# Kernel tuning notes

Hardware: AMD Instinct MI355X
Metric: run time of the kernel (lower is better)

Reference implementation:

```python
import jax, jax.numpy as jnp
from jax import lax
import numpy as np

RADIUS = 2.0
K = 32          # max_neighbors
KNN = 3         # knn_num for FP interpolation
DEPTH = 3
NH = 16         # nhidden
NIN = 16
NOUT = 2
N = 16384
BOX = 32.0


def sqdist(a, b):
    # a: [M,3], b: [N,3] -> [M,N] squared distances (no [M,N,3] intermediate)
    d2 = (jnp.sum(a * a, -1)[:, None] + jnp.sum(b * b, -1)[None, :]
          - 2.0 * a @ b.T)
    return jnp.maximum(d2, 0.0)


def fps(pos, m):
    # farthest point sampling, deterministic start at index 0 (eval mode)
    n = pos.shape[0]
    def step(carry, _):
        mind, last = carry
        d = jnp.sum((pos - pos[last]) ** 2, axis=-1)
        mind = jnp.minimum(mind, d)
        nxt = jnp.argmax(mind).astype(jnp.int32)
        return (mind, nxt), nxt
    init = (jnp.full((n,), jnp.inf, dtype=pos.dtype), jnp.array(0, jnp.int32))
    _, rest = lax.scan(step, init, None, length=m - 1)
    return jnp.concatenate([jnp.zeros((1,), jnp.int32), rest])


def radius_group(pos_tgt, pos_src, r, k):
    # up-to-k neighbors of each target within radius r (nearest-first)
    d2 = sqdist(pos_tgt, pos_src)                      # [M,N]
    neg = jnp.where(d2 <= r * r, -d2, -jnp.inf)
    vals, cols = lax.top_k(neg, k)                     # [M,K]
    valid = jnp.isfinite(vals)
    return cols, valid


def knn_interpolate(x_c, pos_c, pos_f, k):
    d2 = sqdist(pos_f, pos_c)                          # [Nf, Nc]
    negv, nn = lax.top_k(-d2, k)                       # k nearest coarse pts
    w = 1.0 / jnp.maximum(-negv, 1e-16)
    w = w / jnp.sum(w, -1, keepdims=True)
    return jnp.sum(x_c[nn] * w[..., None], axis=1)     # [Nf, C]


def mlp2(h, W0, b0, W1, b1, act_last=True):
    h = jax.nn.relu(h @ W0 + b0)
    h = h @ W1 + b1
    return jax.nn.relu(h) if act_last else h


def setup_inputs() -> dict:
    key = jax.random.key(0)
    ks = jax.random.split(key, 24)
    s = 0.2
    dim_sa = NH + 3   # 19: PointConv concat(x_j, rel_pos)
    dim_fp = NH + NH  # 32: FP concat(interp, skip)
    return {
        "x": jax.random.normal(ks[0], (N, NIN), jnp.float32),
        "pos": jax.random.uniform(ks[1], (N, 3), jnp.float32) * BOX,
        "batch": jnp.zeros((N,), jnp.int32),
        "lin_in_W0": jax.random.normal(ks[2], (NIN, NH)) * s,
        "lin_in_b0": jnp.zeros((NH,), jnp.float32),
        "lin_in_W1": jax.random.normal(ks[3], (NH, NH)) * s,
        "lin_in_b1": jnp.zeros((NH,), jnp.float32),
        "sa_W0": jax.random.normal(ks[4], (DEPTH, dim_sa, dim_sa)) * s,
        "sa_b0": jnp.zeros((DEPTH, dim_sa), jnp.float32),
        "sa_W1": jax.random.normal(ks[5], (DEPTH, dim_sa, NH)) * s,
        "sa_b1": jnp.zeros((DEPTH, NH), jnp.float32),
        "fp_W0": jax.random.normal(ks[6], (DEPTH, dim_fp, dim_fp)) * s,
        "fp_b0": jnp.zeros((DEPTH, dim_fp), jnp.float32),
        "fp_W1": jax.random.normal(ks[7], (DEPTH, dim_fp, NH)) * s,
        "fp_b1": jnp.zeros((DEPTH, NH), jnp.float32),
        "lo_W0": jax.random.normal(ks[8], (NH, NH)) * s,
        "lo_b0": jnp.zeros((NH,), jnp.float32),
        "lo_W1": jax.random.normal(ks[9], (NH, NOUT)) * s,
        "lo_b1": jnp.zeros((NOUT,), jnp.float32),
    }


def reference(x, pos, batch,
              lin_in_W0, lin_in_b0, lin_in_W1, lin_in_b1,
              sa_W0, sa_b0, sa_W1, sa_b1,
              fp_W0, fp_b0, fp_W1, fp_b1,
              lo_W0, lo_b0, lo_W1, lo_b1):
    # lin_in MLP
    h = mlp2(x, lin_in_W0, lin_in_b0, lin_in_W1, lin_in_b1)
    sa = [(h, pos)]
    # SA (downsampling) path
    for i in range(DEPTH):
        xi, pi = sa[i]
        m = pi.shape[0] // 2                      # ratio = 0.5
        idx = fps(pi, m)
        pt = pi[idx]                              # sampled centers [M,3]
        cols, valid = radius_group(pt, pi, RADIUS, K)   # [M,K]
        xj = xi[cols]                             # [M,K,NH]
        rel = pi[cols] - pt[:, None, :]           # [M,K,3]
        msg = jnp.concatenate([xj, rel], -1)      # [M,K,19]
        msg = mlp2(msg, sa_W0[i], sa_b0[i], sa_W1[i], sa_b1[i])
        msg = jnp.where(valid[..., None], msg, -1e30)
        xn = jnp.max(msg, axis=1)                 # max aggregation (PointConv)
        sa.append((xn, pt))
    # FP (upsampling) path
    xf, pf = sa[DEPTH]
    for i in range(DEPTH - 1, -1, -1):
        xs, ps = sa[i]
        xi = knn_interpolate(xf, pf, ps, KNN)
        hcat = jnp.concatenate([xi, xs], -1)      # [Nf, 32]
        xf = mlp2(hcat, fp_W0[i], fp_b0[i], fp_W1[i], fp_b1[i])
        pf = ps
    # lin_out: relu then linear (act=['relu', None])
    return mlp2(xf, lo_W0, lo_b0, lo_W1, lo_b1, act_last=False)
```

## Files before the change

kernel.cpp:

```cpp
#include <hip/hip_runtime.h>
#include <stdint.h>


#define DEV static __device__ __forceinline__

DEV float fadd_(float a, float b){ return __fadd_rn(a,b); }
DEV float fsub_(float a, float b){ return __fsub_rn(a,b); }
DEV float fmul_(float a, float b){ return __fmul_rn(a,b); }
DEV float fdiv_(float a, float b){ return __fdiv_rn(a,b); }

DEV float dot3(float ax,float ay,float az,float bx,float by,float bz){
  return fmaf(az,bz, fmaf(ay,by, __fmul_rn(ax,bx)));
}
DEV float sqd(float na, float nb, float d){
  float t = __fadd_rn(na, nb);
  float u = __fmul_rn(2.0f, d);
  return fmaxf(__fsub_rn(t, u), 0.0f);
}

DEV float d2f_(float ax,float ay,float az,float bx,float by,float bz){
  float dx=fsub_(ax,bx), dy=fsub_(ay,by), dz=fsub_(az,bz);
  return fadd_(fadd_(fmul_(dx,dx),fmul_(dy,dy)),fmul_(dz,dz));
}
DEV float nrm3_(float x,float y,float z){
  return fadd_(fadd_(fmul_(x,x),fmul_(y,y)),fmul_(z,z));
}

DEV float bbd2(float sx,float sy,float sz,
               float lx,float ly,float lz,float hx,float hy,float hz){
  float dx = fmaxf(fmaxf(fsub_(lx,sx), fsub_(sx,hx)), 0.0f);
  float dy = fmaxf(fmaxf(fsub_(ly,sy), fsub_(sy,hy)), 0.0f);
  float dz = fmaxf(fmaxf(fsub_(lz,sz), fsub_(sz,hz)), 0.0f);
  return fadd_(fadd_(fmul_(dx,dx),fmul_(dy,dy)),fmul_(dz,dz));
}

DEV float rfl_f(float v){
  return __int_as_float(__builtin_amdgcn_readfirstlane(__float_as_int(v)));
}

#define DPP0(src, ctrl, rm, bc) \
  __builtin_amdgcn_update_dpp(0, (int)(src), (ctrl), (rm), 0xf, (bc))

#define DPP64(dst, src, ctrl, rm, bc) { \
  uint32_t lo_ = (uint32_t)DPP0((uint32_t)(src), ctrl, rm, bc); \
  uint32_t hi_ = (uint32_t)DPP0((uint32_t)((src)>>32), ctrl, rm, bc); \
  (dst) = (((unsigned long long)hi_)<<32) | lo_; }

#define MERGE4(A1,A2,A3,A4, ctrl, rm, bc) { \
  unsigned long long b1_,b2_,b3_,b4_, m1_,m2_,m3_,m4_, t_; \
  DPP64(b1_, A1, ctrl, rm, bc); \
  DPP64(b2_, A2, ctrl, rm, bc); \
  DPP64(b3_, A3, ctrl, rm, bc); \
  DPP64(b4_, A4, ctrl, rm, bc); \
  m1_ = (A1) > b4_ ? (A1) : b4_; \
  m2_ = (A2) > b3_ ? (A2) : b3_; \
  m3_ = (A3) > b2_ ? (A3) : b2_; \
  m4_ = (A4) > b1_ ? (A4) : b1_; \
  t_ = m1_ < m3_ ? m1_ : m3_;  m1_ = m1_ > m3_ ? m1_ : m3_;  m3_ = t_; \
  t_ = m2_ < m4_ ? m2_ : m4_;  m2_ = m2_ > m4_ ? m2_ : m4_;  m4_ = t_; \
  t_ = m1_ < m2_ ? m1_ : m2_;  m1_ = m1_ > m2_ ? m1_ : m2_;  m2_ = t_; \
  t_ = m3_ < m4_ ? m3_ : m4_;  m3_ = m3_ > m4_ ? m3_ : m4_;  m4_ = t_; \
  (A1)=m1_; (A2)=m2_; (A3)=m3_; (A4)=m4_; }

DEV unsigned long long rdlane64(unsigned long long v, int l){
  uint32_t lo=(uint32_t)__builtin_amdgcn_readlane((int)(uint32_t)v, l);
  uint32_t hi=(uint32_t)__builtin_amdgcn_readlane((int)(uint32_t)(v>>32), l);
  return (((unsigned long long)hi)<<32)|lo;
}

DEV void wtop4(unsigned long long &A1, unsigned long long &A2,
               unsigned long long &A3, unsigned long long &A4){
  MERGE4(A1,A2,A3,A4,0x111,0xf,true)
  MERGE4(A1,A2,A3,A4,0x112,0xf,true)
  MERGE4(A1,A2,A3,A4,0x114,0xf,true)
  MERGE4(A1,A2,A3,A4,0x118,0xf,true)
  MERGE4(A1,A2,A3,A4,0x142,0xa,false)
  MERGE4(A1,A2,A3,A4,0x143,0xc,false)
  A1 = rdlane64(A1,63); A2 = rdlane64(A2,63);
  A3 = rdlane64(A3,63); A4 = rdlane64(A4,63);
}

__global__ __launch_bounds__(256) void k_prep(
    const float* __restrict__ x, const float* __restrict__ pos,
    const float* __restrict__ W0, const float* __restrict__ b0,
    const float* __restrict__ W1, const float* __restrict__ b1,
    float4* __restrict__ pos4, float* __restrict__ h_out, int n)
{
  __shared__ float sW0[256], sb0[16], sW1[256], sb1[16];
  int tid = threadIdx.x;
  sW0[tid] = W0[tid];
  sW1[tid] = W1[tid];
  if (tid < 16){ sb0[tid] = b0[tid]; sb1[tid] = b1[tid]; }
  __syncthreads();
  int p = blockIdx.x*256 + tid;
  if (p >= n) return;

  float px = pos[3*p], py = pos[3*p+1], pz = pos[3*p+2];
  float nrm = fadd_(fadd_(fmul_(px,px), fmul_(py,py)), fmul_(pz,pz));
  pos4[p] = make_float4(px,py,pz,nrm);

  const float4* xr = (const float4*)(x + (size_t)p*16);
  float4 v0 = xr[0], v1 = xr[1], v2 = xr[2], v3 = xr[3];
  float xin[16] = {v0.x,v0.y,v0.z,v0.w, v1.x,v1.y,v1.z,v1.w,
                   v2.x,v2.y,v2.z,v2.w, v3.x,v3.y,v3.z,v3.w};
  float h1[16];
  #pragma unroll
  for (int o=0;o<16;o++){
    float acc = fmul_(xin[0], sW0[o]);
    #pragma unroll
    for (int k=1;k<16;k++) acc = fmaf(xin[k], sW0[k*16+o], acc);
    h1[o] = fmaxf(fadd_(acc, sb0[o]), 0.0f);
  }
  float h2[16];
  #pragma unroll
  for (int o=0;o<16;o++){
    float acc = fmul_(h1[0], sW1[o]);
    #pragma unroll
    for (int k=1;k<16;k++) acc = fmaf(h1[k], sW1[k*16+o], acc);
    h2[o] = fmaxf(fadd_(acc, sb1[o]), 0.0f);
  }
  float4* hw = (float4*)(h_out + (size_t)p*16);
  hw[0] = make_float4(h2[0], h2[1], h2[2], h2[3]);
  hw[1] = make_float4(h2[4], h2[5], h2[6], h2[7]);
  hw[2] = make_float4(h2[8], h2[9], h2[10],h2[11]);
  hw[3] = make_float4(h2[12],h2[13],h2[14],h2[15]);
}

DEV uint32_t expand4(uint32_t v){
  return (v&1u) | ((v&2u)<<2) | ((v&4u)<<4) | ((v&8u)<<6);
}
DEV int cellc(float v){
  int c = (int)(v*0.5f);
  return c < 0 ? 0 : (c > 15 ? 15 : c);
}
DEV uint32_t mkey(float4 p){
  return expand4((uint32_t)cellc(p.x))
       | (expand4((uint32_t)cellc(p.y))<<1)
       | (expand4((uint32_t)cellc(p.z))<<2);
}

__global__ __launch_bounds__(1024) void k_sort(
  const float4* __restrict__ nat, float4* __restrict__ srt,
  int* __restrict__ rank0, int n)
{
  __shared__ uint32_t hist[4096];
  __shared__ uint32_t gsum[1024];
  int tid = threadIdx.x;
  for (int i=tid;i<4096;i+=1024) hist[i]=0u;
  __syncthreads();
  for (int i=tid;i<n;i+=1024){
    float4 p = nat[i];
    atomicAdd(&hist[mkey(p)], 1u);
  }
  __syncthreads();
  uint32_t h0=hist[4*tid],h1=hist[4*tid+1],h2=hist[4*tid+2],h3=hist[4*tid+3];
  gsum[tid] = h0+h1+h2+h3;
  __syncthreads();
  for (int off=1; off<1024; off<<=1){
    uint32_t v = gsum[tid];
    uint32_t a = (tid>=off)? gsum[tid-off] : 0u;
    __syncthreads();
    gsum[tid] = v + a;
    __syncthreads();
  }
  uint32_t excl = (tid>0)? gsum[tid-1] : 0u;
  hist[4*tid]   = excl;
  hist[4*tid+1] = excl + h0;
  hist[4*tid+2] = excl + h0 + h1;
  hist[4*tid+3] = excl + h0 + h1 + h2;
  __syncthreads();
  for (int i=tid;i<n;i+=1024){
    float4 p = nat[i];
    uint32_t r = atomicAdd(&hist[mkey(p)], 1u);
    srt[r] = make_float4(p.x, p.y, p.z, __uint_as_float((uint32_t)i));
    if (i==0) *rank0 = (int)r;
  }
}

template<int P>
__global__ __attribute__((amdgpu_waves_per_eu(4,4)))
__launch_bounds__(1024) void k_fps7(
    const float4* __restrict__ sp4,
    const int* __restrict__ rank0p,
    float4* __restrict__ samp,
    int m)
{
  __shared__ float smind[P*1024];
  __shared__ unsigned long long xch[2][64];
  const int t = threadIdx.x;
  const int lane = t & 63;
  const int w = t >> 6;

  float px[P], py[P], pz[P];
  uint32_t klo[P];
  float blox,bloy,bloz,bhix,bhiy,bhiz;
  #pragma unroll
  for (int k=0;k<P;k++){
    float4 p = sp4[t*P+k];
    px[k]=p.x; py[k]=p.y; pz[k]=p.z;
    uint32_t nat = __float_as_uint(p.w);
    klo[k] = ((0x3FFFu - nat)<<16) | (uint32_t)(t*P+k);
    smind[k*1024+t] = __builtin_inff();
    if (k==0){ blox=bhix=p.x; bloy=bhiy=p.y; bloz=bhiz=p.z; }
    else {
      blox=fminf(blox,p.x); bhix=fmaxf(bhix,p.x);
      bloy=fminf(bloy,p.y); bhiy=fmaxf(bhiy,p.y);
      bloz=fminf(bloz,p.z); bhiz=fmaxf(bhiz,p.z);
    }
  }

  float c0x,c0y,c0z;
  float c1x=0.f,c1y=0.f,c1z=0.f, c2x=0.f,c2y=0.f,c2z=0.f;
  float c3x=0.f,c3y=0.f,c3z=0.f;
  {
    int r0 = *rank0p;
    float4 s0 = sp4[r0];
    c0x=s0.x; c0y=s0.y; c0z=s0.z;
    if (t==0){
      samp[0] = make_float4(s0.x,s0.y,s0.z, nrm3_(s0.x,s0.y,s0.z));
    }
  }
  __syncthreads();

  unsigned long long tc1 = ((unsigned long long)0x7f800000u)<<32;
  unsigned long long tc2 = 0ull, tc3 = 0ull, tc4 = 0ull;
  unsigned long long a1=0ull,a2=0ull,a3=0ull,a4=0ull;

  int u = 1, sel = 1, round = 0;

  while (true){
    float cv = __uint_as_float((uint32_t)(tc1>>32));
    bool act0, act1=false, act2=false, act3=false;
    act0 = fmul_(bbd2(c0x,c0y,c0z, blox,bloy,bloz,bhix,bhiy,bhiz), 0.99999f) < cv;
    if (u>1) act1 = fmul_(bbd2(c1x,c1y,c1z, blox,bloy,bloz,bhix,bhiy,bhiz), 0.99999f) < cv;
    if (u>2) act2 = fmul_(bbd2(c2x,c2y,c2z, blox,bloy,bloz,bhix,bhiy,bhiz), 0.99999f) < cv;
    if (u>3) act3 = fmul_(bbd2(c3x,c3y,c3z, blox,bloy,bloz,bhix,bhiy,bhiz), 0.99999f) < cv;
    bool updp = act0 | act1 | act2 | act3;
    if (__ballot(updp) != 0ull){
      if (updp){
        float nm[P];
        #pragma unroll
        for (int k=0;k<P;k++) nm[k] = smind[k*1024+t];
        if (act0){
          #pragma unroll
          for (int k=0;k<P;k++)
            nm[k] = fminf(nm[k], d2f_(px[k],py[k],pz[k], c0x,c0y,c0z));
        }
        if (u>1){ if (act1){
          #pragma unroll
          for (int k=0;k<P;k++)
            nm[k] = fminf(nm[k], d2f_(px[k],py[k],pz[k], c1x,c1y,c1z));
        }}
        if (u>2){ if (act2){
          #pragma unroll
          for (int k=0;k<P;k++)
            nm[k] = fminf(nm[k], d2f_(px[k],py[k],pz[k], c2x,c2y,c2z));
        }}
        if (u>3){ if (act3){
          #pragma unroll
          for (int k=0;k<P;k++)
            nm[k] = fminf(nm[k], d2f_(px[k],py[k],pz[k], c3x,c3y,c3z));
        }}
        tc1 = 0ull; tc2 = 0ull; tc3 = 0ull; tc4 = 0ull;
        #pragma unroll
        for (int k=0;k<P;k++){
          smind[k*1024+t] = nm[k];
          unsigned long long key =
            (((unsigned long long)__float_as_uint(nm[k]))<<32) | klo[k];
          bool g1_ = key > tc1;
          bool g2_ = key > tc2;
          bool g3_ = key > tc3;
          bool g4_ = key > tc4;
          tc4 = g4_ ? (g3_ ? tc3 : key) : tc4;
          tc3 = g3_ ? (g2_ ? tc2 : key) : tc3;
          tc2 = g2_ ? (g1_ ? tc1 : key) : tc2;
          tc1 = g1_ ? key : tc1;
        }
      }
      a1=tc1; a2=tc2; a3=tc3; a4=tc4;
      wtop4(a1,a2,a3,a4);
    }
    int par = round & 1;
    if (lane < 4){
      unsigned long long pv = (lane==0)?a1:((lane==1)?a2:((lane==2)?a3:a4));
      xch[par][w*4+lane] = pv;
    }
    __syncthreads();
    unsigned long long g1v = xch[par][lane];
    unsigned long long g2v = 0ull, g3v = 0ull, g4v = 0ull;
    wtop4(g1v,g2v,g3v,g4v);
    float4 f1 = sp4[(int)(g1v & 0xFFFFull)];
    float4 f2 = sp4[(int)(g2v & 0xFFFFull)];
    float4 f3 = sp4[(int)(g3v & 0xFFFFull)];
    float4 f4 = sp4[(int)(g4v & 0xFFFFull)];
    float v2 = __uint_as_float((uint32_t)(g2v>>32));
    float v3 = __uint_as_float((uint32_t)(g3v>>32));
    float v4 = __uint_as_float((uint32_t)(g4v>>32));
    float q12 = d2f_(f2.x,f2.y,f2.z, f1.x,f1.y,f1.z);
    bool acc2 = (sel+1 < m) && (q12 >= v2);
    float q13 = d2f_(f3.x,f3.y,f3.z, f1.x,f1.y,f1.z);
    float q23 = d2f_(f3.x,f3.y,f3.z, f2.x,f2.y,f2.z);
    bool acc3 = acc2 && (sel+2 < m) && (fminf(q13,q23) >= v3);
    float q14 = d2f_(f4.x,f4.y,f4.z, f1.x,f1.y,f1.z);
    float q24 = d2f_(f4.x,f4.y,f4.z, f2.x,f2.y,f2.z);
    float q34 = d2f_(f4.x,f4.y,f4.z, f3.x,f3.y,f3.z);
    bool acc4 = acc3 && (sel+3 < m) && (fminf(fminf(q14,q24),q34) >= v4);
    if (t==0)          samp[sel  ] = make_float4(f1.x,f1.y,f1.z, nrm3_(f1.x,f1.y,f1.z));
    if (acc2 && t==1)  samp[sel+1] = make_float4(f2.x,f2.y,f2.z, nrm3_(f2.x,f2.y,f2.z));
    if (acc3 && t==2)  samp[sel+2] = make_float4(f3.x,f3.y,f3.z, nrm3_(f3.x,f3.y,f3.z));
    if (acc4 && t==3)  samp[sel+3] = make_float4(f4.x,f4.y,f4.z, nrm3_(f4.x,f4.y,f4.z));
    int nacc = 1 + (acc2?1:0) + (acc3?1:0) + (acc4?1:0);
    sel += nacc; round++;
    if (sel >= m) break;
    u   = __builtin_amdgcn_readfirstlane(nacc);
    c0x = rfl_f(f1.x); c0y = rfl_f(f1.y); c0z = rfl_f(f1.z);
    c1x = rfl_f(f2.x); c1y = rfl_f(f2.y); c1z = rfl_f(f2.z);
    c2x = rfl_f(f3.x); c2y = rfl_f(f3.y); c2z = rfl_f(f3.z);
    c3x = rfl_f(f4.x); c3y = rfl_f(f4.y); c3z = rfl_f(f4.z);
  }
}

#define SA_CAP 96

__global__ __launch_bounds__(256) void k_sa(
  const float4* __restrict__ spos, int n_src,
  const float4* __restrict__ tpos,
  const float*  __restrict__ F,
  const float* __restrict__ W0, const float* __restrict__ b0,
  const float* __restrict__ W1, const float* __restrict__ b1,
  float* __restrict__ Fout)
{
  __shared__ float sW0[361], sb0[19], sW1[304], sb1[16];
  __shared__ int   nidx[4][SA_CAP];
  __shared__ float nd2[4][SA_CAP];
  int tid = threadIdx.x;
  for (int i=tid;i<361;i+=256) sW0[i]=W0[i];
  for (int i=tid;i<304;i+=256) sW1[i]=W1[i];
  if (tid<19) sb0[tid]=b0[tid];
  if (tid<16) sb1[tid]=b1[tid];
  __syncthreads();

  int wv = tid >> 6, lane = tid & 63;
  int tg = blockIdx.x*4 + wv;
  float4 tp = tpos[tg];

  int cnt = 0;
  for (int base=0; base<n_src; base+=64){
    int j = base + lane;
    float4 sp = spos[j];
    float d2 = sqd(tp.w, sp.w, dot3(tp.x,tp.y,tp.z, sp.x,sp.y,sp.z));
    bool in = (d2 <= 4.0f);
    unsigned long long mk = __ballot(in);
    int pos = cnt + __popcll(mk & ((1ull<<lane)-1ull));
    if (in && pos < SA_CAP){ nidx[wv][pos]=j; nd2[wv][pos]=d2; }
    cnt += __popcll(mk);
  }
  if (cnt > SA_CAP) cnt = SA_CAP;

  if (cnt > 32){
    uint64_t tk0=0, tk1=0;
    for (int r=0;r<32;r++){
      float bvv = 3.5e38f; int bii = 0x7fffffff; int be = 0;
      for (int e=0;e<cnt;e++){
        bool done = (e<64) ? ((tk0>>e)&1ull) : ((tk1>>(e-64))&1ull);
        if (done) continue;
        float dv = nd2[wv][e]; int di = nidx[wv][e];
        if (dv < bvv || (dv == bvv && di < bii)){ bvv=dv; bii=di; be=e; }
      }
      if (be < 64) tk0 |= (1ull<<be); else tk1 |= (1ull<<(be-64));
    }
    int myi = 0; float myd = 0.0f;
    if (lane < 32){
      int seen = 0, sel = -1;
      for (int e=0;e<cnt && sel<0;e++){
        bool s = (e<64) ? ((tk0>>e)&1ull) : ((tk1>>(e-64))&1ull);
        if (s){ if (seen == lane) sel = e; seen++; }
      }
      myi = nidx[wv][sel]; myd = nd2[wv][sel];
    }
    __builtin_amdgcn_wave_barrier();
    if (lane < 32){ nidx[wv][lane]=myi; nd2[wv][lane]=myd; }
    __builtin_amdgcn_wave_barrier();
    cnt = 32;
  }

  float in19[19];
  #pragma unroll
  for (int k=0;k<19;k++) in19[k] = 0.0f;
  if (lane < cnt){
    int j = nidx[wv][lane];
    const float4* fr = (const float4*)(F + (size_t)j*16);
    float4 a=fr[0], b=fr[1], c=fr[2], d=fr[3];
    in19[0]=a.x; in19[1]=a.y; in19[2]=a.z; in19[3]=a.w;
    in19[4]=b.x; in19[5]=b.y; in19[6]=b.z; in19[7]=b.w;
    in19[8]=c.x; in19[9]=c.y; in19[10]=c.z; in19[11]=c.w;
    in19[12]=d.x; in19[13]=d.y; in19[14]=d.z; in19[15]=d.w;
    float4 sp = spos[j];
    in19[16]=fsub_(sp.x,tp.x); in19[17]=fsub_(sp.y,tp.y); in19[18]=fsub_(sp.z,tp.z);
  }
  float h[19];
  #pragma unroll
  for (int o=0;o<19;o++){
    float acc = fmul_(in19[0], sW0[o]);
    #pragma unroll
    for (int k=1;k<19;k++) acc = fmaf(in19[k], sW0[k*19+o], acc);
    h[o] = fmaxf(fadd_(acc, sb0[o]), 0.0f);
  }
  float outv[16];
  #pragma unroll
  for (int o=0;o<16;o++){
    float acc = fmul_(h[0], sW1[o]);
    #pragma unroll
    for (int k=1;k<19;k++) acc = fmaf(h[k], sW1[k*16+o], acc);
    float v = fmaxf(fadd_(acc, sb1[o]), 0.0f);
    outv[o] = (lane < cnt) ? v : -1e30f;
  }
  #pragma unroll
  for (int o=0;o<16;o++){
    float v = outv[o];
    #pragma unroll
    for (int s=1;s<64;s<<=1) v = fmaxf(v, __shfl_xor(v, s));
    outv[o] = v;
  }
  if (lane == 0){
    float4* dst = (float4*)(Fout + (size_t)tg*16);
    dst[0] = make_float4(outv[0], outv[1], outv[2], outv[3]);
    dst[1] = make_float4(outv[4], outv[5], outv[6], outv[7]);
    dst[2] = make_float4(outv[8], outv[9], outv[10],outv[11]);
    dst[3] = make_float4(outv[12],outv[13],outv[14],outv[15]);
  }
}

__global__ __launch_bounds__(256) void k_fp(
  const float4* __restrict__ fpos,
  const float4* __restrict__ cpos, int n_coarse,
  const float* __restrict__ Fc, const float* __restrict__ Fs,
  const float* __restrict__ W0, const float* __restrict__ b0,
  const float* __restrict__ W1, const float* __restrict__ b1,
  const float* __restrict__ loW0, const float* __restrict__ lob0,
  const float* __restrict__ loW1, const float* __restrict__ lob1,
  float* __restrict__ outp, int final_)
{
  __shared__ float sW0[1024], sb0[32], sW1[512], sb1[16];
  __shared__ float sLW0[256], sLb0[16], sLW1[32], sLb1[2];
  int tid = threadIdx.x;
  for (int i=tid;i<1024;i+=256) sW0[i]=W0[i];
  for (int i=tid;i<512;i+=256)  sW1[i]=W1[i];
  if (tid<32) sb0[tid]=b0[tid];
  if (tid<16) sb1[tid]=b1[tid];
  if (final_){
    sLW0[tid & 255] = loW0[tid & 255];
    if (tid<16) sLb0[tid]=lob0[tid];
    if (tid<32) sLW1[tid]=loW1[tid];
    if (tid<2)  sLb1[tid]=lob1[tid];
  }
  __syncthreads();

  int wv = tid >> 6, lane = tid & 63;
  int f = blockIdx.x*4 + wv;
  float4 fp = fpos[f];

  float c0v=3.5e38f, c1v=3.5e38f, c2v=3.5e38f;
  int   c0i=0x7fffffff, c1i=0x7fffffff, c2i=0x7fffffff;
  for (int j=lane; j<n_coarse; j+=64){
    float4 cp = cpos[j];
    float d2 = sqd(fp.w, cp.w, dot3(fp.x,fp.y,fp.z, cp.x,cp.y,cp.z));
    if (d2 < c2v || (d2 == c2v && j < c2i)){
      bool a0 = (d2 < c0v) || (d2 == c0v && j < c0i);
      bool a1 = (d2 < c1v) || (d2 == c1v && j < c1i);
      c2v = a1 ? c1v : d2;               c2i = a1 ? c1i : j;
      c1v = a0 ? c0v : (a1 ? d2 : c1v);  c1i = a0 ? c0i : (a1 ? j : c1i);
      c0v = a0 ? d2 : c0v;               c0i = a0 ? j  : c0i;
    }
  }
  float nnd[3]; int nni[3];
  #pragma unroll
  for (int r=0;r<3;r++){
    float v = c0v; int idx = c0i;
    #pragma unroll
    for (int s=1;s<64;s<<=1){
      float ov = __shfl_xor(v, s);
      int   oi = __shfl_xor(idx, s);
      bool tk = (ov < v) || (ov == v && oi < idx);
      v = tk ? ov : v; idx = tk ? oi : idx;
    }
    nnd[r] = v; nni[r] = idx;
    if (c0v == v && c0i == idx){
      c0v=c1v; c0i=c1i; c1v=c2v; c1i=c2i; c2v=3.5e38f; c2i=0x7fffffff;
    }
  }
  float w0 = fdiv_(1.0f, fmaxf(nnd[0], 1e-16f));
  float w1 = fdiv_(1.0f, fmaxf(nnd[1], 1e-16f));
  float w2 = fdiv_(1.0f, fmaxf(nnd[2], 1e-16f));
  float ws = fadd_(fadd_(w0,w1),w2);
  w0 = fdiv_(w0,ws); w1 = fdiv_(w1,ws); w2 = fdiv_(w2,ws);

  float hv = 0.0f;
  if (lane < 16){
    int c = lane;
    float x0 = Fc[(size_t)nni[0]*16 + c];
    float x1 = Fc[(size_t)nni[1]*16 + c];
    float x2 = Fc[(size_t)nni[2]*16 + c];
    hv = fadd_(fadd_(fmul_(w0,x0), fmul_(w1,x1)), fmul_(w2,x2));
  } else if (lane < 32){
    hv = Fs[(size_t)f*16 + (lane-16)];
  }
  int o1 = lane & 31;
  float acc = fmul_(__shfl(hv, 0), sW0[o1]);
  #pragma unroll
  for (int k=1;k<32;k++) acc = fmaf(__shfl(hv, k), sW0[k*32+o1], acc);
  float g1 = fmaxf(fadd_(acc, sb0[o1]), 0.0f);
  int o2 = lane & 15;
  float a2 = fmul_(__shfl(g1, 0), sW1[o2]);
  #pragma unroll
  for (int k=1;k<32;k++) a2 = fmaf(__shfl(g1, k), sW1[k*16+o2], a2);
  float g2 = fmaxf(fadd_(a2, sb1[o2]), 0.0f);

  if (!final_){
    if (lane < 16) outp[(size_t)f*16 + lane] = g2;
  } else {
    float a3 = fmul_(__shfl(g2, 0), sLW0[o2]);
    #pragma unroll
    for (int k=1;k<16;k++) a3 = fmaf(__shfl(g2, k), sLW0[k*16+o2], a3);
    float q = fmaxf(fadd_(a3, sLb0[o2]), 0.0f);
    int o3 = lane & 1;
    float a4 = fmul_(__shfl(q, 0), sLW1[o3]);
    #pragma unroll
    for (int k=1;k<16;k++) a4 = fmaf(__shfl(q, k), sLW1[k*2+o3], a4);
    a4 = fadd_(a4, sLb1[o3]);
    if (lane < 2) outp[(size_t)f*2 + lane] = a4;
  }
}

extern "C" void kernel_launch(void* const* d_in, const int* in_sizes, int n_in,
                              void* d_out, int out_size, void* d_ws, size_t ws_size,
                              hipStream_t stream) {
  (void)in_sizes; (void)n_in; (void)out_size; (void)ws_size;
  const float* x     = (const float*)d_in[0];
  const float* pos   = (const float*)d_in[1];
  const float* liW0  = (const float*)d_in[3];
  const float* lib0  = (const float*)d_in[4];
  const float* liW1  = (const float*)d_in[5];
  const float* lib1  = (const float*)d_in[6];
  const float* saW0  = (const float*)d_in[7];
  const float* sab0  = (const float*)d_in[8];
  const float* saW1  = (const float*)d_in[9];
  const float* sab1  = (const float*)d_in[10];
  const float* fpW0  = (const float*)d_in[11];
  const float* fpb0  = (const float*)d_in[12];
  const float* fpW1  = (const float*)d_in[13];
  const float* fpb1  = (const float*)d_in[14];
  const float* loW0  = (const float*)d_in[15];
  const float* lob0  = (const float*)d_in[16];
  const float* loW1  = (const float*)d_in[17];
  const float* lob1  = (const float*)d_in[18];
  float* out = (float*)d_out;

  char* ws = (char*)d_ws;
  size_t off = 0;
  auto alloc = [&](size_t bytes)->void* {
    void* p = ws + off;
    off += (bytes + 255) & ~(size_t)255;
    return p;
  };
  float4* P0 = (float4*)alloc(16384u*16);
  float4* P1 = (float4*)alloc(8192u*16);
  float4* P2 = (float4*)alloc(4096u*16);
  float4* P3 = (float4*)alloc(2048u*16);
  float*  F0 = (float*)alloc(16384u*16*4);
  float*  F1 = (float*)alloc(8192u*16*4);
  float*  F2 = (float*)alloc(4096u*16*4);
  float*  F3 = (float*)alloc(2048u*16*4);
  float*  G2 = (float*)alloc(4096u*16*4);
  float*  G1 = (float*)alloc(8192u*16*4);
  float4* S0 = (float4*)alloc(16384u*16);
  float4* S1 = (float4*)alloc(8192u*16);
  float4* S2 = (float4*)alloc(4096u*16);
  int*    R0 = (int*)alloc(256);

  k_prep<<<64,256,0,stream>>>(x,pos, liW0,lib0,liW1,lib1, P0,F0, 16384);

  k_sort<<<1,1024,0,stream>>>(P0, S0, R0+0, 16384);
  k_fps7<16><<<1,1024,0,stream>>>(S0, R0+0, P1, 8192);
  k_sa<<<2048,256,0,stream>>>(P0,16384, P1, F0, saW0,      sab0,    saW1,      sab1,    F1);
  k_sort<<<1,1024,0,stream>>>(P1, S1, R0+1, 8192);
  k_fps7<8><<<1,1024,0,stream>>>(S1, R0+1, P2, 4096);
  k_sa<<<1024,256,0,stream>>>(P1, 8192, P2, F1, saW0+361,  sab0+19, saW1+304,  sab1+16, F2);
  k_sort<<<1,1024,0,stream>>>(P2, S2, R0+2, 4096);
  k_fps7<4><<<1,1024,0,stream>>>(S2, R0+2, P3, 2048);
  k_sa<<< 512,256,0,stream>>>(P2, 4096, P3, F2, saW0+722,  sab0+38, saW1+608,  sab1+32, F3);

  k_fp<<<1024,256,0,stream>>>(P2, P3,2048, F3, F2,
      fpW0+2048, fpb0+64, fpW1+1024, fpb1+32,
      loW0,lob0,loW1,lob1, G2, 0);
  k_fp<<<2048,256,0,stream>>>(P1, P2,4096, G2, F1,
      fpW0+1024, fpb0+32, fpW1+512,  fpb1+16,
      loW0,lob0,loW1,lob1, G1, 0);
  k_fp<<<4096,256,0,stream>>>(P0, P1,8192, G1, F0,
      fpW0,      fpb0,    fpW1,      fpb1,
      loW0,lob0,loW1,lob1, out, 1);
}
```

Baseline: 21.66 ms.

## Keep FPS min-distances in registers and centralize final top-4 selection in wave 0

The farthest-point-sampling kernel now keeps each thread's per-point minimum distances in registers instead of reading and writing them through shared memory on every update. The cross-wave top-4 merge is no longer done redundantly by all 16 waves. Wave 0 alone merges the 16 per-wave candidate lists, fetches the winning points, runs the acceptance tests and writes the samples. It then broadcasts the chosen centres through a small shared buffer. This removes shared-memory traffic and redundant gathers and reductions in the serial loop. The cost is a second barrier per round and more register pressure.

New measurement: 25.27 ms. +16.7%, slower.

```diff
diff --git a/kernel.cpp b/kernel.cpp
--- a/kernel.cpp
+++ b/kernel.cpp
@@ -80,6 +80,16 @@
   A3 = rdlane64(A3,63); A4 = rdlane64(A4,63);
 }
 
+DEV void qtop4(unsigned long long &A1, unsigned long long &A2,
+               unsigned long long &A3, unsigned long long &A4){
+  MERGE4(A1,A2,A3,A4,0x111,0xf,true)
+  MERGE4(A1,A2,A3,A4,0x112,0xf,true)
+  MERGE4(A1,A2,A3,A4,0x114,0xf,true)
+  MERGE4(A1,A2,A3,A4,0x118,0xf,true)
+  A1 = rdlane64(A1,15); A2 = rdlane64(A2,15);
+  A3 = rdlane64(A3,15); A4 = rdlane64(A4,15);
+}
+
 __global__ __launch_bounds__(256) void k_prep(
     const float* __restrict__ x, const float* __restrict__ pos,
     const float* __restrict__ W0, const float* __restrict__ b0,
@@ -179,28 +189,28 @@
 
 template<int P>
 __global__ __attribute__((amdgpu_waves_per_eu(4,4)))
-__launch_bounds__(1024) void k_fps7(
+__launch_bounds__(1024) void k_fps8(
     const float4* __restrict__ sp4,
     const int* __restrict__ rank0p,
     float4* __restrict__ samp,
     int m)
 {
-  __shared__ float smind[P*1024];
-  __shared__ unsigned long long xch[2][64];
+  __shared__ __attribute__((aligned(16))) unsigned long long xch[64];
+  __shared__ __attribute__((aligned(16))) float4 gb4[4];
   const int t = threadIdx.x;
   const int lane = t & 63;
   const int w = t >> 6;
 
-  float px[P], py[P], pz[P];
+  float px[P], py[P], pz[P], mind[P];
   uint32_t klo[P];
   float blox,bloy,bloz,bhix,bhiy,bhiz;
   #pragma unroll
   for (int k=0;k<P;k++){
     float4 p = sp4[t*P+k];
     px[k]=p.x; py[k]=p.y; pz[k]=p.z;
+    mind[k] = __builtin_inff();
     uint32_t nat = __float_as_uint(p.w);
     klo[k] = ((0x3FFFu - nat)<<16) | (uint32_t)(t*P+k);
-    smind[k*1024+t] = __builtin_inff();
     if (k==0){ blox=bhix=p.x; bloy=bhiy=p.y; bloz=bhiz=p.z; }
     else {
       blox=fminf(blox,p.x); bhix=fmaxf(bhix,p.x);
@@ -224,9 +234,8 @@
 
   unsigned long long tc1 = ((unsigned long long)0x7f800000u)<<32;
   unsigned long long tc2 = 0ull, tc3 = 0ull, tc4 = 0ull;
-  unsigned long long a1=0ull,a2=0ull,a3=0ull,a4=0ull;
-
-  int u = 1, sel = 1, round = 0;
+
+  int u = 1, sel = 1;
 
   while (true){
     float cv = __uint_as_float((uint32_t)(tc1>>32));
@@ -238,35 +247,31 @@
     bool updp = act0 | act1 | act2 | act3;
     if (__ballot(updp) != 0ull){
       if (updp){
-        float nm[P];
-        #pragma unroll
-        for (int k=0;k<P;k++) nm[k] = smind[k*1024+t];
         if (act0){
           #pragma unroll
           for (int k=0;k<P;k++)
-            nm[k] = fminf(nm[k], d2f_(px[k],py[k],pz[k], c0x,c0y,c0z));
+            mind[k] = fminf(mind[k], d2f_(px[k],py[k],pz[k], c0x,c0y,c0z));
         }
         if (u>1){ if (act1){
           #pragma unroll
           for (int k=0;k<P;k++)
-            nm[k] = fminf(nm[k], d2f_(px[k],py[k],pz[k], c1x,c1y,c1z));
+            mind[k] = fminf(mind[k], d2f_(px[k],py[k],pz[k], c1x,c1y,c1z));
         }}
         if (u>2){ if (act2){
           #pragma unroll
           for (int k=0;k<P;k++)
-            nm[k] = fminf(nm[k], d2f_(px[k],py[k],pz[k], c2x,c2y,c2z));
+            mind[k] = fminf(mind[k], d2f_(px[k],py[k],pz[k], c2x,c2y,c2z));
         }}
         if (u>3){ if (act3){
           #pragma unroll
           for (int k=0;k<P;k++)
-            nm[k] = fminf(nm[k], d2f_(px[k],py[k],pz[k], c3x,c3y,c3z));
+            mind[k] = fminf(mind[k], d2f_(px[k],py[k],pz[k], c3x,c3y,c3z));
         }}
         tc1 = 0ull; tc2 = 0ull; tc3 = 0ull; tc4 = 0ull;
         #pragma unroll
         for (int k=0;k<P;k++){
-          smind[k*1024+t] = nm[k];
           unsigned long long key =
-            (((unsigned long long)__float_as_uint(nm[k]))<<32) | klo[k];
+            (((unsigned long long)__float_as_uint(mind[k]))<<32) | klo[k];
           bool g1_ = key > tc1;
           bool g2_ = key > tc2;
           bool g3_ = key > tc3;
@@ -277,46 +282,60 @@
           tc1 = g1_ ? key : tc1;
         }
       }
-      a1=tc1; a2=tc2; a3=tc3; a4=tc4;
+      unsigned long long a1=tc1, a2=tc2, a3=tc3, a4=tc4;
       wtop4(a1,a2,a3,a4);
-    }
-    int par = round & 1;
-    if (lane < 4){
-      unsigned long long pv = (lane==0)?a1:((lane==1)?a2:((lane==2)?a3:a4));
-      xch[par][w*4+lane] = pv;
+      if (lane < 4){
+        unsigned long long pv = (lane==0)?a1:((lane==1)?a2:((lane==2)?a3:a4));
+        xch[w*4+lane] = pv;
+      }
     }
     __syncthreads();
-    unsigned long long g1v = xch[par][lane];
-    unsigned long long g2v = 0ull, g3v = 0ull, g4v = 0ull;
-    wtop4(g1v,g2v,g3v,g4v);
-    float4 f1 = sp4[(int)(g1v & 0xFFFFull)];
-    float4 f2 = sp4[(int)(g2v & 0xFFFFull)];
-    float4 f3 = sp4[(int)(g3v & 0xFFFFull)];
-    float4 f4 = sp4[(int)(g4v & 0xFFFFull)];
-    float v2 = __uint_as_float((uint32_t)(g2v>>32));
-    float v3 = __uint_as_float((uint32_t)(g3v>>32));
-    float v4 = __uint_as_float((uint32_t)(g4v>>32));
-    float q12 = d2f_(f2.x,f2.y,f2.z, f1.x,f1.y,f1.z);
-    bool acc2 = (sel+1 < m) && (q12 >= v2);
-    float q13 = d2f_(f3.x,f3.y,f3.z, f1.x,f1.y,f1.z);
-    float q23 = d2f_(f3.x,f3.y,f3.z, f2.x,f2.y,f2.z);
-    bool acc3 = acc2 && (sel+2 < m) && (fminf(q13,q23) >= v3);
-    float q14 = d2f_(f4.x,f4.y,f4.z, f1.x,f1.y,f1.z);
-    float q24 = d2f_(f4.x,f4.y,f4.z, f2.x,f2.y,f2.z);
-    float q34 = d2f_(f4.x,f4.y,f4.z, f3.x,f3.y,f3.z);
-    bool acc4 = acc3 && (sel+3 < m) && (fminf(fminf(q14,q24),q34) >= v4);
-    if (t==0)          samp[sel  ] = make_float4(f1.x,f1.y,f1.z, nrm3_(f1.x,f1.y,f1.z));
-    if (acc2 && t==1)  samp[sel+1] = make_float4(f2.x,f2.y,f2.z, nrm3_(f2.x,f2.y,f2.z));
-    if (acc3 && t==2)  samp[sel+2] = make_float4(f3.x,f3.y,f3.z, nrm3_(f3.x,f3.y,f3.z));
-    if (acc4 && t==3)  samp[sel+3] = make_float4(f4.x,f4.y,f4.z, nrm3_(f4.x,f4.y,f4.z));
-    int nacc = 1 + (acc2?1:0) + (acc3?1:0) + (acc4?1:0);
-    sel += nacc; round++;
+    if (w == 0){
+      unsigned long long A1=0ull,A2=0ull,A3=0ull,A4=0ull;
+      if (lane < 16){
+        const unsigned long long* b = &xch[lane*4];
+        A1=b[0]; A2=b[1]; A3=b[2]; A4=b[3];
+      }
+      qtop4(A1,A2,A3,A4);
+      float4 f1 = sp4[(int)(A1 & 0xFFFFull)];
+      float4 f2 = sp4[(int)(A2 & 0xFFFFull)];
+      float4 f3 = sp4[(int)(A3 & 0xFFFFull)];
+      float4 f4 = sp4[(int)(A4 & 0xFFFFull)];
+      float v2 = __uint_as_float((uint32_t)(A2>>32));
+      float v3 = __uint_as_float((uint32_t)(A3>>32));
+      float v4 = __uint_as_float((uint32_t)(A4>>32));
+      float q12 = d2f_(f2.x,f2.y,f2.z, f1.x,f1.y,f1.z);
+      bool acc2 = (sel+1 < m) && (q12 >= v2);
+      float q13 = d2f_(f3.x,f3.y,f3.z, f1.x,f1.y,f1.z);
+      float q23 = d2f_(f3.x,f3.y,f3.z, f2.x,f2.y,f2.z);
+      bool acc3 = acc2 && (sel+2 < m) && (fminf(q13,q23) >= v3);
+      float q14 = d2f_(f4.x,f4.y,f4.z, f1.x,f1.y,f1.z);
+      float q24 = d2f_(f4.x,f4.y,f4.z, f2.x,f2.y,f2.z);
+      float q34 = d2f_(f4.x,f4.y,f4.z, f3.x,f3.y,f3.z);
+      bool acc4 = acc3 && (sel+3 < m) && (fminf(fminf(q14,q24),q34) >= v4);
+      if (lane==0)          samp[sel  ] = make_float4(f1.x,f1.y,f1.z, nrm3_(f1.x,f1.y,f1.z));
+      if (acc2 && lane==1)  samp[sel+1] = make_float4(f2.x,f2.y,f2.z, nrm3_(f2.x,f2.y,f2.z));
+      if (acc3 && lane==2)  samp[sel+2] = make_float4(f3.x,f3.y,f3.z, nrm3_(f3.x,f3.y,f3.z));
+      if (acc4 && lane==3)  samp[sel+3] = make_float4(f4.x,f4.y,f4.z, nrm3_(f4.x,f4.y,f4.z));
+      int nacc = 1 + (acc2?1:0) + (acc3?1:0) + (acc4?1:0);
+      if (lane < 4){
+        float fx = (lane==0)?f1.x:((lane==1)?f2.x:((lane==2)?f3.x:f4.x));
+        float fy = (lane==0)?f1.y:((lane==1)?f2.y:((lane==2)?f3.y:f4.y));
+        float fz = (lane==0)?f1.z:((lane==1)?f2.z:((lane==2)?f3.z:f4.z));
+        float fw = (lane==0)?__int_as_float(nacc):0.0f;
+        gb4[lane] = make_float4(fx,fy,fz,fw);
+      }
+    }
+    __syncthreads();
+    float4 r0 = gb4[0], r1 = gb4[1], r2 = gb4[2], r3 = gb4[3];
+    int nacc = __float_as_int(r0.w);
+    sel += nacc;
     if (sel >= m) break;
     u   = __builtin_amdgcn_readfirstlane(nacc);
-    c0x = rfl_f(f1.x); c0y = rfl_f(f1.y); c0z = rfl_f(f1.z);
-    c1x = rfl_f(f2.x); c1y = rfl_f(f2.y); c1z = rfl_f(f2.z);
-    c2x = rfl_f(f3.x); c2y = rfl_f(f3.y); c2z = rfl_f(f3.z);
-    c3x = rfl_f(f4.x); c3y = rfl_f(f4.y); c3z = rfl_f(f4.z);
+    c0x = rfl_f(r0.x); c0y = rfl_f(r0.y); c0z = rfl_f(r0.z);
+    c1x = rfl_f(r1.x); c1y = rfl_f(r1.y); c1z = rfl_f(r1.z);
+    c2x = rfl_f(r2.x); c2y = rfl_f(r2.y); c2z = rfl_f(r2.z);
+    c3x = rfl_f(r3.x); c3y = rfl_f(r3.y); c3z = rfl_f(r3.z);
   }
 }
 
@@ -581,13 +600,13 @@
   k_prep<<<64,256,0,stream>>>(x,pos, liW0,lib0,liW1,lib1, P0,F0, 16384);
 
   k_sort<<<1,1024,0,stream>>>(P0, S0, R0+0, 16384);
-  k_fps7<16><<<1,1024,0,stream>>>(S0, R0+0, P1, 8192);
+  k_fps8<16><<<1,1024,0,stream>>>(S0, R0+0, P1, 8192);
   k_sa<<<2048,256,0,stream>>>(P0,16384, P1, F0, saW0,      sab0,    saW1,      sab1,    F1);
   k_sort<<<1,1024,0,stream>>>(P1, S1, R0+1, 8192);
-  k_fps7<8><<<1,1024,0,stream>>>(S1, R0+1, P2, 4096);
+  k_fps8<8><<<1,1024,0,stream>>>(S1, R0+1, P2, 4096);
   k_sa<<<1024,256,0,stream>>>(P1, 8192, P2, F1, saW0+361,  sab0+19, saW1+304,  sab1+16, F2);
   k_sort<<<1,1024,0,stream>>>(P2, S2, R0+2, 4096);
-  k_fps7<4><<<1,1024,0,stream>>>(S2, R0+2, P3, 2048);
+  k_fps8<4><<<1,1024,0,stream>>>(S2, R0+2, P3, 2048);
   k_sa<<< 512,256,0,stream>>>(P2, 4096, P3, F2, saW0+722,  sab0+38, saW1+608,  sab1+32, F3);
 
   k_fp<<<1024,256,0,stream>>>(P2, P3,2048, F3, F2,
```
